# Kernel tuning notes

Measured on AMD Instinct MI355X. Metric: run time of the kernel, lower is better.

Reference implementation:

```python
import jax, jax.numpy as jnp
import numpy as np

B, L, H, V = 256, 200, 128, 50000
NLAYER, K = 2, 20
NEG = -1e10


def setup_inputs() -> dict:
    key = jax.random.key(0)
    ks = jax.random.split(key, 14)
    lens = jax.random.randint(ks[0], (B,), 50, L + 1)
    pos = jnp.arange(L)
    valid = pos[None, :] < lens[:, None]                       # [B,L] bool
    seq = jnp.where(valid, jax.random.randint(ks[1], (B, L), 1, V), 0)
    lengths = valid.astype(jnp.int32)                          # >0 where real token
    reverse_lengths = jnp.where(valid, lens[:, None] - pos[None, :], 0)  # 1..len, 0=pad

    def nrm(k, shape, s=0.02):
        return jax.random.normal(k, shape, jnp.float32) * s

    emb_w = nrm(ks[2], (V, H)).at[0].set(0.0)
    wnoise_w = nrm(ks[3], (L + 1, H)).at[0].set(0.0)
    cluster_w = nrm(ks[4], (L + 1, 1)).at[0].set(0.0)
    ffn1_w = nrm(ks[5], (H, H), 0.05)
    ffn1_b = jnp.zeros((H,), jnp.float32)
    ffn2_w = nrm(ks[6], (H, H), 0.05)
    ffn2_b = jnp.zeros((H,), jnp.float32)
    ln_g = jnp.ones((H,), jnp.float32)
    ln_b = jnp.zeros((H,), jnp.float32)
    gate_w = nrm(ks[7], (2 * H, H), 0.05)
    coff = jax.random.normal(ks[8], (NLAYER, B, L, L), jnp.float32)  # fixed noise (torch.normal)
    return dict(seq=seq, lengths=lengths, reverse_lengths=reverse_lengths,
                emb_w=emb_w, wnoise_w=wnoise_w, cluster_w=cluster_w,
                ffn1_w=ffn1_w, ffn1_b=ffn1_b, ffn2_w=ffn2_w, ffn2_b=ffn2_b,
                ln_g=ln_g, ln_b=ln_b, gate_w=gate_w, coff=coff)


def _sp(x):  # torch.nn.Softplus(threshold=1): identity above 1
    return jnp.where(x > 1.0, x, jnp.log1p(jnp.exp(jnp.minimum(x, 1.0))))


def _forward(seq, lengths, reverse_lengths, emb_w, wnoise_w, cluster_w,
             ffn1_w, ffn1_b, ffn2_w, ffn2_b, ln_g, ln_b, gate_w, coff):
    b, l = seq.shape
    mask = (lengths > 0).astype(jnp.float32)                   # [B,L]
    hidden = emb_w[seq]                                        # [B,L,H]
    slen = jnp.sum(mask, axis=1)                               # [B]
    e_s = hidden[jnp.arange(b), (slen - 1).astype(jnp.int32)]  # last real token state
    zero_layer = jnp.sum(hidden, 1) / slen[:, None]
    layer_collect = [zero_layer]
    eye = jnp.eye(l, dtype=hidden.dtype)
    pair_ok = mask[:, :, None] * mask[:, None, :]              # [B,L,L]
    for i in range(coff.shape[0]):
        wn = wnoise_w[reverse_lengths]                         # [B,L,H]
        sim = jnp.einsum('bld,bmd->blm', hidden, hidden)
        nrm = jnp.linalg.norm(hidden, axis=2, keepdims=True)   # [B,L,1]
        sim = sim / (nrm * nrm.transpose(0, 2, 1) + 1e-6)      # cosine similarity
        diag = cluster_w[reverse_lengths][..., 0]              # [B,L]
        sim = sim + diag[:, :, None] * eye                     # diag_embed add
        sim = sim + coff[i] * _sp(jnp.einsum('bld,bmd->blm', hidden, wn))
        msim = jnp.where(pair_ok == 0.0, NEG, sim)             # masked_fill
        _, idx = jax.lax.top_k(msim, K)                        # [B,L,K]
        sel = jnp.zeros_like(msim).at[jnp.arange(b)[:, None, None],
                                      jnp.arange(l)[None, :, None], idx].set(1.0)
        edges = sel * (msim > NEG).astype(msim.dtype)          # top-k & above-threshold
        cluster_label = edges.transpose(0, 2, 1)
        sim_softmax = jax.nn.softmax(msim, axis=2)
        ssm = cluster_label * sim_softmax                      # [B,L,L] sparse-weighted
        update_hidden = jnp.einsum('blm,bmd->bld', ssm, hidden)
        cmask = jnp.sum(ssm, axis=2)                           # [B,L]
        cmask = cmask / jnp.maximum(jnp.linalg.norm(cmask, axis=1, keepdims=True), 1e-12)
        if i > 0:
            update_hidden = update_hidden * (slen > 1.0).astype(hidden.dtype)[:, None, None]
        feed1 = jax.nn.relu(update_hidden @ ffn1_w + ffn1_b)
        pre = feed1 @ ffn2_w + ffn2_b + update_hidden          # dropout = identity (eval)
        mu = jnp.mean(pre, -1, keepdims=True)
        var = jnp.var(pre, -1, keepdims=True)
        feed2 = (pre - mu) / jnp.sqrt(var + 1e-5) * ln_g + ln_b
        layer_collect.append(jnp.sum(feed2 * cmask[:, :, None], 1))
    e_c = jnp.mean(jnp.stack(layer_collect, 1), 1)             # [B,H]
    alpha = jax.nn.sigmoid(jnp.concatenate([e_c, e_s], -1) @ gate_w)
    sess = alpha * e_c + (1.0 - alpha) * e_s
    scores = sess @ emb_w.T                                    # [B,V]
    return scores


def reference(seq, lengths, reverse_lengths, emb_w, wnoise_w, cluster_w,
              ffn1_w, ffn1_b, ffn2_w, ffn2_b, ln_g, ln_b, gate_w, coff):
    scores = _forward(seq, lengths, reverse_lengths, emb_w, wnoise_w, cluster_w,
                      ffn1_w, ffn1_b, ffn2_w, ffn2_b, ln_g, ln_b, gate_w, coff)
    return (scores, jnp.asarray(0.0, jnp.float32))  # con_loss == 0 when abs=True
```

## Files before the change

kernel.cpp:

```cpp
#include <hip/hip_runtime.h>
#include <cstdint>
#include <cstddef>

namespace {
constexpr int B = 256, L = 200, H = 128, V = 50000, TK = 20;
constexpr int NT = 1563;
constexpr float NEGV = -1e10f;
}

using bf16x8 = __attribute__((ext_vector_type(8))) short;
using s16x8  = __attribute__((ext_vector_type(8))) short;
using f32x16 = __attribute__((ext_vector_type(16))) float;

__device__ inline unsigned short f2bf(float f) {
  unsigned int u = __float_as_uint(f);
  unsigned int r = (u + 0x7fffu + ((u >> 16) & 1u)) >> 16;
  return (unsigned short)r;
}

#define DPP_QUAD_XOR1 0xB1
#define DPP_QUAD_XOR2 0x4E
#define DPP_ROW_HMIRR 0x141
#define DPP_ROW_MIRR  0x140

template <int CTRL>
__device__ inline unsigned dpp16_max_step(unsigned v) {
  unsigned t = (unsigned)__builtin_amdgcn_update_dpp(0, (int)v, CTRL, 0xF, 0xF, true);
  return v > t ? v : t;
}
__device__ inline unsigned grp16_max(unsigned v) {
  v = dpp16_max_step<DPP_QUAD_XOR1>(v);
  v = dpp16_max_step<DPP_QUAD_XOR2>(v);
  v = dpp16_max_step<DPP_ROW_HMIRR>(v);
  v = dpp16_max_step<DPP_ROW_MIRR>(v);
  return v;
}
template <int CTRL>
__device__ inline float dpp16_add_step(float v) {
  int t = __builtin_amdgcn_update_dpp(0, __float_as_int(v), CTRL, 0xF, 0xF, true);
  return v + __int_as_float(t);
}
__device__ inline float grp16_sum(float v) {
  v = dpp16_add_step<DPP_QUAD_XOR1>(v);
  v = dpp16_add_step<DPP_QUAD_XOR2>(v);
  v = dpp16_add_step<DPP_ROW_HMIRR>(v);
  v = dpp16_add_step<DPP_ROW_MIRR>(v);
  return v;
}

__device__ inline unsigned f2key(float f) {
  unsigned b = __float_as_uint(f);
  unsigned m = (unsigned)((int)b >> 31);
  return b ^ (m | 0x80000000u);
}
__device__ inline float key2f(unsigned u) {
  unsigned b = (u & 0x80000000u) ? (u & 0x7fffffffu) : ~u;
  return __uint_as_float(b);
}

__global__ __launch_bounds__(256) void k_embed(const int* __restrict__ seq,
                                               const int* __restrict__ rev,
                                               const float* __restrict__ emb,
                                               const float* __restrict__ wnoise,
                                               float* __restrict__ hidden,
                                               float* __restrict__ nrm,
                                               s16x8* __restrict__ hbh,
                                               s16x8* __restrict__ hbl,
                                               s16x8* __restrict__ wnh,
                                               s16x8* __restrict__ wnl) {
  int b = blockIdx.x / 7, lt = blockIdx.x % 7;
  int t = threadIdx.x;
  int r = t >> 3, c2 = t & 7;
  int l = lt * 32 + r;
  bool valid = l < L;
  float vv[16], wv[16];
  if (valid) {
    int row = b * L + l;
    int tok = seq[row];
    const float4* ep = (const float4*)&emb[(size_t)tok * H + c2 * 16];
    const float4* wp = (const float4*)&wnoise[(size_t)rev[row] * H + c2 * 16];
#pragma unroll
    for (int i = 0; i < 4; ++i) {
      float4 x = ep[i];
      vv[i * 4 + 0] = x.x; vv[i * 4 + 1] = x.y; vv[i * 4 + 2] = x.z; vv[i * 4 + 3] = x.w;
      float4 y = wp[i];
      wv[i * 4 + 0] = y.x; wv[i * 4 + 1] = y.y; wv[i * 4 + 2] = y.z; wv[i * 4 + 3] = y.w;
    }
  } else {
#pragma unroll
    for (int i = 0; i < 16; ++i) { vv[i] = 0.f; wv[i] = 0.f; }
  }
  if (valid) {
    int row = b * L + l;
#pragma unroll
    for (int i = 0; i < 4; ++i)
      *(float4*)&hidden[(size_t)row * H + c2 * 16 + i * 4] =
          make_float4(vv[i * 4], vv[i * 4 + 1], vv[i * 4 + 2], vv[i * 4 + 3]);
    float s = 0.f;
#pragma unroll
    for (int i = 0; i < 16; ++i) s += vv[i] * vv[i];
    s += __shfl_down(s, 4, 8);
    s += __shfl_down(s, 2, 8);
    s += __shfl_down(s, 1, 8);
    if (c2 == 0) nrm[row] = sqrtf(s);
  }
  s16x8 h0, h1, l0, l1, w0, w1, x0, x1;
#pragma unroll
  for (int i = 0; i < 8; ++i) {
    unsigned short hi = f2bf(vv[i]);
    h0[i] = (short)hi;
    l0[i] = (short)f2bf(vv[i] - __uint_as_float((unsigned)hi << 16));
    unsigned short wh = f2bf(wv[i]);
    w0[i] = (short)wh;
    x0[i] = (short)f2bf(wv[i] - __uint_as_float((unsigned)wh << 16));
  }
#pragma unroll
  for (int i = 0; i < 8; ++i) {
    unsigned short hi = f2bf(vv[8 + i]);
    h1[i] = (short)hi;
    l1[i] = (short)f2bf(vv[8 + i] - __uint_as_float((unsigned)hi << 16));
    unsigned short wh = f2bf(wv[8 + i]);
    w1[i] = (short)wh;
    x1[i] = (short)f2bf(wv[8 + i] - __uint_as_float((unsigned)wh << 16));
  }
  size_t fi0 = ((size_t)(b * 7 + lt) * 8 + c2) * 64 + r;
  size_t fi1 = fi0 + 32;
  hbh[fi0] = h0; hbh[fi1] = h1;
  hbl[fi0] = l0; hbl[fi1] = l1;
  wnh[fi0] = w0; wnh[fi1] = w1;
  wnl[fi0] = x0; wnl[fi1] = x1;
}

__global__ __launch_bounds__(512) void k_init(const int* __restrict__ lengths,
                                              const float* __restrict__ hidden,
                                              float* __restrict__ ecacc,
                                              float* __restrict__ e_s) {
  int b = blockIdx.x, tid = threadIdx.x;
  __shared__ float part[4][128];
  __shared__ int wcnt[8];
  __shared__ int s_slen;
  int c = (tid < L && lengths[b * L + tid] > 0) ? 1 : 0;
  for (int o = 32; o > 0; o >>= 1) c += __shfl_down(c, o, 64);
  if ((tid & 63) == 0) wcnt[tid >> 6] = c;
  __syncthreads();
  if (tid == 0) {
    int s = 0;
#pragma unroll
    for (int i = 0; i < 8; ++i) s += wcnt[i];
    s_slen = s;
  }
  int h = tid & 127, seg = tid >> 7;
  float s = 0.f;
  for (int l = seg; l < L; l += 4) s += hidden[(size_t)(b * L + l) * H + h];
  part[seg][h] = s;
  __syncthreads();
  if (tid < 128) {
    float tot = part[0][h] + part[1][h] + part[2][h] + part[3][h];
    int slen = s_slen;
    ecacc[b * H + h] = tot / (float)slen;
    e_s[b * H + h] = hidden[(size_t)(b * L + slen - 1) * H + h];
  }
}

__global__ __launch_bounds__(256) void k_simws(const s16x8* __restrict__ hbh,
                                               const s16x8* __restrict__ hbl,
                                               const s16x8* __restrict__ wnh,
                                               const s16x8* __restrict__ wnl,
                                               const float* __restrict__ nrm,
                                               const int* __restrict__ rev,
                                               const float* __restrict__ cluster,
                                               float* __restrict__ S0,
                                               float* __restrict__ WS) {
  int orig = blockIdx.x;
  int xcd = orig & 7, slot = orig >> 3;
  int b = xcd * 32 + slot / 7, lt = slot % 7;
  int wid = threadIdx.x >> 6, lane = threadIdx.x & 63;
  int lr = lane & 31, kh = lane >> 5;
  size_t abase = ((size_t)(b * 7 + lt) * 8) * 64 + lane;
  bf16x8 ah[8], al[8];
#pragma unroll
  for (int ks = 0; ks < 8; ++ks) {
    ah[ks] = (bf16x8)hbh[abase + ks * 64];
    al[ks] = (bf16x8)hbl[abase + ks * 64];
  }
  for (int mt = wid; mt < 7; mt += 4) {
    size_t bbase = ((size_t)(b * 7 + mt) * 8) * 64 + lane;
    f32x16 accs = {}, accw = {};
#pragma unroll
    for (int ks = 0; ks < 8; ++ks) {
      bf16x8 bhh = (bf16x8)hbh[bbase + ks * 64];
      bf16x8 bhl = (bf16x8)hbl[bbase + ks * 64];
      bf16x8 bwh = (bf16x8)wnh[bbase + ks * 64];
      bf16x8 bwl = (bf16x8)wnl[bbase + ks * 64];
      accs = __builtin_amdgcn_mfma_f32_32x32x16_bf16(ah[ks], bhh, accs, 0, 0, 0);
      accs = __builtin_amdgcn_mfma_f32_32x32x16_bf16(ah[ks], bhl, accs, 0, 0, 0);
      accs = __builtin_amdgcn_mfma_f32_32x32x16_bf16(al[ks], bhh, accs, 0, 0, 0);
      accw = __builtin_amdgcn_mfma_f32_32x32x16_bf16(ah[ks], bwh, accw, 0, 0, 0);
      accw = __builtin_amdgcn_mfma_f32_32x32x16_bf16(ah[ks], bwl, accw, 0, 0, 0);
      accw = __builtin_amdgcn_mfma_f32_32x32x16_bf16(al[ks], bwh, accw, 0, 0, 0);
    }
    int m = mt * 32 + lr;
    if (m < L) {
      float nm = nrm[b * L + m];
#pragma unroll
      for (int r = 0; r < 16; ++r) {
        int row = lt * 32 + (r & 3) + 8 * (r >> 2) + 4 * kh;
        if (row < L) {
          float nl = nrm[b * L + row];
          float s0 = accs[r] * __builtin_amdgcn_rcpf(nl * nm + 1e-6f);
          if (row == m) s0 += cluster[rev[b * L + row]];
          size_t o = (size_t)(b * L + row) * L + m;
          S0[o] = s0;
          float x = accw[r];
          WS[o] = (x > 1.f) ? x : __logf(1.f + __expf(x));
        }
      }
    }
  }
}

__global__ __launch_bounds__(256) void k_rowpass(const float* __restrict__ S0,
                                                 const float* __restrict__ WS,
                                                 const float* __restrict__ coff_i,
                                                 const int* __restrict__ lengths,
                                                 float* __restrict__ P,
                                                 unsigned char* __restrict__ ET) {
  int wid = threadIdx.x >> 6, lane = threadIdx.x & 63;
  int g = lane >> 4, q = lane & 15;
  int bb = blockIdx.x / 13, blk = blockIdx.x % 13;
  int l = blk * 16 + wid * 4 + g;
  bool lvalid = l < L;
  int lrow = bb * L + (lvalid ? l : 0);
  bool mask_l = lvalid && (lengths[lrow] > 0);
  size_t base = (size_t)lrow * L;
  float val[13]; unsigned key[13]; unsigned vmask = 0;
#pragma unroll
  for (int j = 0; j < 13; ++j) {
    int m = q + 16 * j;
    float v = 0.f; bool ok = false;
    if (mask_l && m < L) {
      ok = lengths[bb * L + m] > 0;
      if (ok) v = S0[base + m] + coff_i[base + m] * WS[base + m];
    }
    val[j] = v;
    key[j] = ok ? f2key(v) : 0u;
    vmask |= ok ? (1u << j) : 0u;
  }
  unsigned Mu = 0u;
  for (int t = 0; t < TK; ++t) {
    unsigned lv = key[0]; int lj = 0;
#pragma unroll
    for (int j = 1; j < 13; ++j) {
      bool gt = key[j] > lv;
      lv = gt ? key[j] : lv;
      lj = gt ? j : lj;
    }
    unsigned gm = grp16_max(lv);
    if (t == 0) Mu = gm;
    if (__all(gm == 0u)) break;
    unsigned long long bal = __ballot(lv == gm && gm != 0u);
    unsigned long long mine = bal & (0xFFFFull << (g * 16));
    int owner = mine ? (int)__builtin_ctzll(mine) : -1;
    bool is_owner = (lane == owner);
    if (is_owner) {
      int m = q + 16 * lj;
      ET[((size_t)bb * L + m) * L + l] = 1;
    }
#pragma unroll
    for (int j = 0; j < 13; ++j) key[j] = (is_owner && lj == j) ? 0u : key[j];
  }
  float M = key2f(Mu);
  float e[13]; float s = 0.f;
#pragma unroll
  for (int j = 0; j < 13; ++j) {
    float ev = ((vmask >> j) & 1u) ? __expf(val[j] - M) : 0.f;
    e[j] = ev; s += ev;
  }
  s = grp16_sum(s);
  float inv = (s > 0.f) ? __builtin_amdgcn_rcpf(s) : 0.f;
  if (lvalid) {
#pragma unroll
    for (int j = 0; j < 13; ++j) {
      int m = q + 16 * j;
      if (m < L) P[base + m] = e[j] * inv;
    }
  }
}

__global__ __launch_bounds__(256) void k_compact(float* __restrict__ P,
                                                 unsigned char* __restrict__ ET,
                                                 float* __restrict__ cmask,
                                                 int* __restrict__ cnt) {
  int wid = threadIdx.x >> 6, lane = threadIdx.x & 63;
  int row = blockIdx.x * 4 + wid;
  size_t base = (size_t)row * L;
  float w[4];
  float s = 0.f;
#pragma unroll
  for (int j = 0; j < 4; ++j) {
    int m = lane + 64 * j;
    float ww = 0.f;
    if (m < L) ww = P[base + m] * (float)ET[base + m];
    w[j] = ww; s += ww;
  }
  float ssum = s;
  for (int off = 1; off < 64; off <<= 1) ssum += __shfl_xor(ssum, off, 64);
  if (lane == 0) cmask[row] = ssum;
  int pos_base = 0;
#pragma unroll
  for (int j = 0; j < 4; ++j) {
    bool nz = (w[j] != 0.f);
    unsigned long long mk = __ballot(nz);
    int rank = __popcll(mk & ((1ull << lane) - 1ull));
    if (nz) {
      int pos = pos_base + rank;
      ET[base + pos] = (unsigned char)(lane + 64 * j);
      P[base + pos] = w[j];
    }
    pos_base += (int)__popcll(mk);
  }
  if (lane == 0) cnt[row] = pos_base;
}

__global__ __launch_bounds__(64) void k_cnorm(float* __restrict__ cmask) {
  int b = blockIdx.x, lane = threadIdx.x;
  float v[4]; float s = 0.f;
#pragma unroll
  for (int j = 0; j < 4; ++j) {
    int l = lane + 64 * j;
    float x = (l < L) ? cmask[b * L + l] : 0.f;
    v[j] = x; s += x * x;
  }
  for (int off = 1; off < 64; off <<= 1) s += __shfl_xor(s, off, 64);
  float inv = 1.f / fmaxf(sqrtf(s), 1e-12f);
#pragma unroll
  for (int j = 0; j < 4; ++j) {
    int l = lane + 64 * j;
    if (l < L) cmask[b * L + l] = v[j] * inv;
  }
}

__global__ __launch_bounds__(256) void k_update(const float* __restrict__ P,
                                                const unsigned char* __restrict__ ET,
                                                const int* __restrict__ cnt,
                                                const float* __restrict__ hidden,
                                                float* __restrict__ upd) {
  int row = blockIdx.x * 2 + (threadIdx.x >> 7);
  int h = threadIdx.x & 127;
  int b = row / L;
  size_t base = (size_t)row * L;
  int n = cnt[row];
  float acc = 0.f;
  for (int e0 = 0; e0 < n; e0 += TK) {
    float w[TK]; int m[TK];
    float4 p4[5];
#pragma unroll
    for (int i = 0; i < 5; ++i) p4[i] = *(const float4*)&P[base + e0 + i * 4];
#pragma unroll
    for (int i = 0; i < 5; ++i) {
      w[i * 4 + 0] = p4[i].x; w[i * 4 + 1] = p4[i].y;
      w[i * 4 + 2] = p4[i].z; w[i * 4 + 3] = p4[i].w;
    }
#pragma unroll
    for (int e = 0; e < TK; ++e) m[e] = ET[base + e0 + e];
    float hv[TK];
#pragma unroll
    for (int e = 0; e < TK; ++e)
      hv[e] = hidden[(size_t)(b * L + m[e]) * H + h];
#pragma unroll
    for (int e = 0; e < TK; ++e)
      acc += ((e0 + e) < n ? w[e] : 0.f) * hv[e];
  }
  upd[(size_t)row * H + h] = acc;
}

__global__ __launch_bounds__(256) void k_ffn(float* __restrict__ upd,
                                             const float* __restrict__ W1,
                                             const float* __restrict__ b1,
                                             const float* __restrict__ W2,
                                             const float* __restrict__ b2,
                                             const float* __restrict__ g,
                                             const float* __restrict__ beta,
                                             const float* __restrict__ cmask) {
  constexpr int AS = 136;
  __shared__ __align__(16) char smem[4 * 64 * AS * 2];
  short* ahs = (short*)smem;
  short* als = ahs + 64 * AS;
  short* f1h = (short*)(smem + 2 * 64 * AS * 2);
  short* f1l = f1h + 64 * AS;
  float (*ps)[132] = (float (*)[132])smem;
  __shared__ float mus[64], rsd[64];
  int row0 = blockIdx.x * 64;
  int tid = threadIdx.x;
  int wid = tid >> 6, lane = tid & 63;
  int lr = lane & 31, kh = lane >> 5;
  int n0 = wid * 32;
  int n = n0 + lr;
#pragma unroll
  for (int it = 0; it < 8; ++it) {
    int f = it * 256 + tid;
    int r = f >> 5, c4 = (f & 31) * 4;
    float4 v = *(const float4*)&upd[(size_t)(row0 + r) * H + c4];
    float vv[4] = {v.x, v.y, v.z, v.w};
    unsigned short hh[4]; short ll[4];
#pragma unroll
    for (int q2 = 0; q2 < 4; ++q2) {
      hh[q2] = f2bf(vv[q2]);
      ll[q2] = (short)f2bf(vv[q2] - __uint_as_float((unsigned)hh[q2] << 16));
    }
    uint2 ph = make_uint2((unsigned)hh[0] | ((unsigned)hh[1] << 16),
                          (unsigned)hh[2] | ((unsigned)hh[3] << 16));
    uint2 pl = make_uint2((unsigned short)ll[0] | ((unsigned)(unsigned short)ll[1] << 16),
                          (unsigned short)ll[2] | ((unsigned)(unsigned short)ll[3] << 16));
    *(uint2*)&ahs[r * AS + c4] = ph;
    *(uint2*)&als[r * AS + c4] = pl;
  }
  __syncthreads();
  bf16x8 wfh[8], wfl[8];
#pragma unroll
  for (int ks = 0; ks < 8; ++ks) {
#pragma unroll
    for (int i = 0; i < 8; ++i) {
      float w = W1[(size_t)(ks * 16 + kh * 8 + i) * H + n];
      unsigned short hi = f2bf(w);
      wfh[ks][i] = (short)hi;
      wfl[ks][i] = (short)f2bf(w - __uint_as_float((unsigned)hi << 16));
    }
  }
  f32x16 acc0, acc1;
  {
    float bv = b1[n];
#pragma unroll
    for (int r = 0; r < 16; ++r) { acc0[r] = bv; acc1[r] = bv; }
  }
#pragma unroll
  for (int ks = 0; ks < 8; ++ks) {
    bf16x8 xh0 = *(const bf16x8*)&ahs[(0 * 32 + lr) * AS + ks * 16 + kh * 8];
    bf16x8 xl0 = *(const bf16x8*)&als[(0 * 32 + lr) * AS + ks * 16 + kh * 8];
    bf16x8 xh1 = *(const bf16x8*)&ahs[(1 * 32 + lr) * AS + ks * 16 + kh * 8];
    bf16x8 xl1 = *(const bf16x8*)&als[(1 * 32 + lr) * AS + ks * 16 + kh * 8];
    acc0 = __builtin_amdgcn_mfma_f32_32x32x16_bf16(xh0, wfh[ks], acc0, 0, 0, 0);
    acc0 = __builtin_amdgcn_mfma_f32_32x32x16_bf16(xl0, wfh[ks], acc0, 0, 0, 0);
    acc0 = __builtin_amdgcn_mfma_f32_32x32x16_bf16(xh0, wfl[ks], acc0, 0, 0, 0);
    acc1 = __builtin_amdgcn_mfma_f32_32x32x16_bf16(xh1, wfh[ks], acc1, 0, 0, 0);
    acc1 = __builtin_amdgcn_mfma_f32_32x32x16_bf16(xl1, wfh[ks], acc1, 0, 0, 0);
    acc1 = __builtin_amdgcn_mfma_f32_32x32x16_bf16(xh1, wfl[ks], acc1, 0, 0, 0);
  }
#pragma unroll
  for (int r = 0; r < 16; ++r) {
    int crow = (r & 3) + 8 * (r >> 2) + 4 * kh;
    float f0 = fmaxf(acc0[r], 0.f);
    unsigned short h0 = f2bf(f0);
    f1h[crow * AS + n] = (short)h0;
    f1l[crow * AS + n] = (short)f2bf(f0 - __uint_as_float((unsigned)h0 << 16));
    float f1v = fmaxf(acc1[r], 0.f);
    unsigned short h1 = f2bf(f1v);
    f1h[(32 + crow) * AS + n] = (short)h1;
    f1l[(32 + crow) * AS + n] = (short)f2bf(f1v - __uint_as_float((unsigned)h1 << 16));
  }
  __syncthreads();
#pragma unroll
  for (int ks = 0; ks < 8; ++ks) {
#pragma unroll
    for (int i = 0; i < 8; ++i) {
      float w = W2[(size_t)(ks * 16 + kh * 8 + i) * H + n];
      unsigned short hi = f2bf(w);
      wfh[ks][i] = (short)hi;
      wfl[ks][i] = (short)f2bf(w - __uint_as_float((unsigned)hi << 16));
    }
  }
  {
    float bv = b2[n];
#pragma unroll
    for (int r = 0; r < 16; ++r) { acc0[r] = bv; acc1[r] = bv; }
  }
#pragma unroll
  for (int ks = 0; ks < 8; ++ks) {
    bf16x8 xh0 = *(const bf16x8*)&f1h[(0 * 32 + lr) * AS + ks * 16 + kh * 8];
    bf16x8 xl0 = *(const bf16x8*)&f1l[(0 * 32 + lr) * AS + ks * 16 + kh * 8];
    bf16x8 xh1 = *(const bf16x8*)&f1h[(1 * 32 + lr) * AS + ks * 16 + kh * 8];
    bf16x8 xl1 = *(const bf16x8*)&f1l[(1 * 32 + lr) * AS + ks * 16 + kh * 8];
    acc0 = __builtin_amdgcn_mfma_f32_32x32x16_bf16(xh0, wfh[ks], acc0, 0, 0, 0);
    acc0 = __builtin_amdgcn_mfma_f32_32x32x16_bf16(xl0, wfh[ks], acc0, 0, 0, 0);
    acc0 = __builtin_amdgcn_mfma_f32_32x32x16_bf16(xh0, wfl[ks], acc0, 0, 0, 0);
    acc1 = __builtin_amdgcn_mfma_f32_32x32x16_bf16(xh1, wfh[ks], acc1, 0, 0, 0);
    acc1 = __builtin_amdgcn_mfma_f32_32x32x16_bf16(xl1, wfh[ks], acc1, 0, 0, 0);
    acc1 = __builtin_amdgcn_mfma_f32_32x32x16_bf16(xh1, wfl[ks], acc1, 0, 0, 0);
  }
#pragma unroll
  for (int r = 0; r < 16; ++r) {
    int crow = (r & 3) + 8 * (r >> 2) + 4 * kh;
    float p0 = acc0[r] + upd[(size_t)(row0 + crow) * H + n];
    float p1 = acc1[r] + upd[(size_t)(row0 + 32 + crow) * H + n];
    acc0[r] = p0; acc1[r] = p1;
    ps[crow][n] = p0;
    ps[32 + crow][n] = p1;
  }
  __syncthreads();
  {
    int r = tid >> 2, sub = tid & 3;
    float s = 0.f, sq = 0.f;
#pragma unroll
    for (int j = 0; j < 8; ++j) {
      float4 x = *(const float4*)&ps[r][sub * 32 + j * 4];
      s += x.x + x.y + x.z + x.w;
      sq += x.x * x.x + x.y * x.y + x.z * x.z + x.w * x.w;
    }
    s += __shfl_down(s, 2, 4);  s += __shfl_down(s, 1, 4);
    sq += __shfl_down(sq, 2, 4); sq += __shfl_down(sq, 1, 4);
    if (sub == 0) {
      float mu = s * (1.f / 128.f);
      float var = sq * (1.f / 128.f) - mu * mu;
      mus[r] = mu;
      rsd[r] = rsqrtf(var + 1e-5f);
    }
  }
  __syncthreads();
  {
    float gn = g[n], bn = beta[n];
#pragma unroll
    for (int r = 0; r < 16; ++r) {
      int crow = (r & 3) + 8 * (r >> 2) + 4 * kh;
      float o0 = ((acc0[r] - mus[crow]) * rsd[crow] * gn + bn) * cmask[row0 + crow];
      float o1 = ((acc1[r] - mus[32 + crow]) * rsd[32 + crow] * gn + bn) * cmask[row0 + 32 + crow];
      upd[(size_t)(row0 + crow) * H + n] = o0;
      upd[(size_t)(row0 + 32 + crow) * H + n] = o1;
    }
  }
}

__global__ __launch_bounds__(512) void k_ecadd(const float* __restrict__ wf,
                                               float* __restrict__ ecacc) {
  int b = blockIdx.x, tid = threadIdx.x;
  __shared__ float part[4][128];
  int h = tid & 127, seg = tid >> 7;
  float s = 0.f;
  for (int l = seg; l < L; l += 4) s += wf[(size_t)(b * L + l) * H + h];
  part[seg][h] = s;
  __syncthreads();
  if (tid < 128)
    ecacc[b * H + h] += part[0][h] + part[1][h] + part[2][h] + part[3][h];
}

__global__ __launch_bounds__(256) void k_embconv(const float* __restrict__ emb,
                                                 s16x8* __restrict__ ebh,
                                                 s16x8* __restrict__ ebl) {
  int nt = blockIdx.x;
  int t = threadIdx.x;
  int r = t >> 3, c2 = t & 7;
  int n = nt * 32 + r;
  float vv[16];
  if (n < V) {
    const float4* ep = (const float4*)&emb[(size_t)n * H + c2 * 16];
#pragma unroll
    for (int i = 0; i < 4; ++i) {
      float4 x = ep[i];
      vv[i * 4 + 0] = x.x; vv[i * 4 + 1] = x.y; vv[i * 4 + 2] = x.z; vv[i * 4 + 3] = x.w;
    }
  } else {
#pragma unroll
    for (int i = 0; i < 16; ++i) vv[i] = 0.f;
  }
  s16x8 h0, h1, l0, l1;
#pragma unroll
  for (int i = 0; i < 8; ++i) {
    unsigned short hi = f2bf(vv[i]);
    h0[i] = (short)hi;
    l0[i] = (short)f2bf(vv[i] - __uint_as_float((unsigned)hi << 16));
    unsigned short hj = f2bf(vv[8 + i]);
    h1[i] = (short)hj;
    l1[i] = (short)f2bf(vv[8 + i] - __uint_as_float((unsigned)hj << 16));
  }
  size_t fi0 = ((size_t)nt * 8 + c2) * 64 + r;
  size_t fi1 = fi0 + 32;
  ebh[fi0] = h0; ebh[fi1] = h1;
  ebl[fi0] = l0; ebl[fi1] = l1;
}

__global__ __launch_bounds__(128) void k_gate(const float* __restrict__ ecacc,
                                              const float* __restrict__ e_s,
                                              const float* __restrict__ gw,
                                              float* __restrict__ sess,
                                              float* __restrict__ out) {
  __shared__ float cat[256];
  int b = blockIdx.x, h = threadIdx.x;
  float ec = ecacc[b * H + h] * (1.f / 3.f);
  float es = e_s[b * H + h];
  cat[h] = ec; cat[128 + h] = es;
  __syncthreads();
  float a = 0.f;
  for (int j = 0; j < 256; ++j) a = fmaf(cat[j], gw[(size_t)j * H + h], a);
  a = 1.f / (1.f + __expf(-a));
  sess[b * H + h] = a * ec + (1.f - a) * es;
  if (b == 0 && h == 0) out[(size_t)B * V] = 0.f;
}

__global__ __launch_bounds__(256) void k_scores(const float* __restrict__ sess,
                                                const s16x8* __restrict__ ebh,
                                                const s16x8* __restrict__ ebl,
                                                float* __restrict__ out) {
  int wid = threadIdx.x >> 6, lane = threadIdx.x & 63;
  int lr = lane & 31, kh = lane >> 5;
  int mt = blockIdx.y;
  int m = mt * 32 + lr;
  bf16x8 ah[8], al[8];
#pragma unroll
  for (int ks = 0; ks < 8; ++ks) {
    const float* sp = &sess[(size_t)m * H + ks * 16 + kh * 8];
    float4 a = *(const float4*)sp;
    float4 c = *(const float4*)(sp + 4);
    float av[8] = {a.x, a.y, a.z, a.w, c.x, c.y, c.z, c.w};
#pragma unroll
    for (int i = 0; i < 8; ++i) {
      unsigned short hi = f2bf(av[i]);
      ah[ks][i] = (short)hi;
      al[ks][i] = (short)f2bf(av[i] - __uint_as_float((unsigned)hi << 16));
    }
  }
  int ntEnd = min(blockIdx.x * 16 + 16, NT);
  for (int nt = blockIdx.x * 16 + wid; nt < ntEnd; nt += 4) {
    size_t bbase = ((size_t)nt * 8) * 64 + lane;
    f32x16 acc = {};
#pragma unroll
    for (int ks = 0; ks < 8; ++ks) {
      bf16x8 bh = (bf16x8)ebh[bbase + ks * 64];
      bf16x8 bl = (bf16x8)ebl[bbase + ks * 64];
      acc = __builtin_amdgcn_mfma_f32_32x32x16_bf16(ah[ks], bh, acc, 0, 0, 0);
      acc = __builtin_amdgcn_mfma_f32_32x32x16_bf16(al[ks], bh, acc, 0, 0, 0);
      acc = __builtin_amdgcn_mfma_f32_32x32x16_bf16(ah[ks], bl, acc, 0, 0, 0);
    }
    int n = nt * 32 + lr;
    if (n < V) {
#pragma unroll
      for (int r = 0; r < 16; ++r) {
        int row = mt * 32 + (r & 3) + 8 * (r >> 2) + 4 * kh;
        out[(size_t)row * V + n] = acc[r];
      }
    }
  }
}

extern "C" void kernel_launch(void* const* d_in, const int* in_sizes, int n_in,
                              void* d_out, int out_size, void* d_ws, size_t ws_size,
                              hipStream_t stream) {
  const int*   seq  = (const int*)d_in[0];
  const int*   lens = (const int*)d_in[1];
  const int*   rev  = (const int*)d_in[2];
  const float* emb  = (const float*)d_in[3];
  const float* wnz  = (const float*)d_in[4];
  const float* clw  = (const float*)d_in[5];
  const float* w1   = (const float*)d_in[6];
  const float* fb1  = (const float*)d_in[7];
  const float* w2   = (const float*)d_in[8];
  const float* fb2  = (const float*)d_in[9];
  const float* lng  = (const float*)d_in[10];
  const float* lnb  = (const float*)d_in[11];
  const float* gw   = (const float*)d_in[12];
  const float* coff = (const float*)d_in[13];
  float* out = (float*)d_out;

  char* ws = (char*)d_ws;
  size_t off = 0;
  auto alloc = [&](size_t bytes) {
    void* p = ws + off;
    off += (bytes + 255) & ~(size_t)255;
    return p;
  };
  float* hidden = (float*)alloc((size_t)B * L * H * 4);
  float* nrm    = (float*)alloc((size_t)B * L * 4);
  float* S0     = (float*)alloc((size_t)B * L * L * 4);
  float* WS     = (float*)alloc((size_t)B * L * L * 4);
  float* P      = (float*)alloc((size_t)B * L * L * 4);
  float* upd    = (float*)alloc((size_t)B * L * H * 4);
  float* cmask  = (float*)alloc((size_t)B * L * 4);
  int*   cnt    = (int*)alloc((size_t)B * L * 4);
  float* e_s    = (float*)alloc((size_t)B * H * 4);
  float* ecacc  = (float*)alloc((size_t)B * H * 4);
  float* sess   = (float*)alloc((size_t)B * H * 4);
  unsigned char* ET = (unsigned char*)alloc((size_t)B * L * L);
  s16x8* hbh = (s16x8*)alloc((size_t)B * 7 * 8 * 64 * 16);
  s16x8* wnh = (s16x8*)alloc((size_t)B * 7 * 8 * 64 * 16);
  s16x8* hbl = (s16x8*)P;
  s16x8* wnl = (s16x8*)upd;
  s16x8* ebh = (s16x8*)S0;
  s16x8* ebl = (s16x8*)WS;

  k_embed<<<B * 7, 256, 0, stream>>>(seq, rev, emb, wnz, hidden, nrm,
                                     hbh, hbl, wnh, wnl);
  k_init<<<B, 512, 0, stream>>>(lens, hidden, ecacc, e_s);
  k_simws<<<B * 7, 256, 0, stream>>>(hbh, hbl, wnh, wnl, nrm, rev, clw, S0, WS);

  for (int i = 0; i < 2; ++i) {
    hipMemsetAsync(ET, 0, (size_t)B * L * L, stream);
    k_rowpass<<<B * 13, 256, 0, stream>>>(S0, WS, coff + (size_t)i * B * L * L,
                                          lens, P, ET);
    k_compact<<<B * L / 4, 256, 0, stream>>>(P, ET, cmask, cnt);
    k_cnorm<<<B, 64, 0, stream>>>(cmask);
    k_update<<<B * L / 2, 256, 0, stream>>>(P, ET, cnt, hidden, upd);
    k_ffn<<<B * L / 64, 256, 0, stream>>>(upd, w1, fb1, w2, fb2, lng, lnb, cmask);
    k_ecadd<<<B, 512, 0, stream>>>(upd, ecacc);
  }

  k_embconv<<<NT, 256, 0, stream>>>(emb, ebh, ebl);
  k_gate<<<B, 128, 0, stream>>>(ecacc, e_s, gw, sess, out);
  k_scores<<<dim3((NT + 15) / 16, 8), 256, 0, stream>>>(sess, ebh, ebl, out);
}
```

Baseline: 475.3 us.

## Fuse similarity/weight computation with per-row top-k softmax for both layers

Merges the similarity/softplus MFMA kernel with the row pass so the S0 and WS tiles stay in shared memory instead of round-tripping through global memory. The row pass for both layers is computed up front in the fused kernel, writing separate P and ET buffers per layer, and both ET buffers are zeroed before the loop. This removes two full B*L*L float writes and several reads plus kernel launches, at the cost of about 53KB of shared memory per block (lower occupancy) and a serialized top-k phase inside the MFMA kernel. Workspace aliasing is reshuffled to fit the extra buffers.

```diff
diff --git a/kernel.cpp b/kernel.cpp
--- a/kernel.cpp
+++ b/kernel.cpp
@@ -162,15 +162,21 @@
   }
 }
 
-__global__ __launch_bounds__(256) void k_simws(const s16x8* __restrict__ hbh,
+__global__ __launch_bounds__(256) void k_fused(const s16x8* __restrict__ hbh,
                                                const s16x8* __restrict__ hbl,
                                                const s16x8* __restrict__ wnh,
                                                const s16x8* __restrict__ wnl,
                                                const float* __restrict__ nrm,
                                                const int* __restrict__ rev,
                                                const float* __restrict__ cluster,
-                                               float* __restrict__ S0,
-                                               float* __restrict__ WS) {
+                                               const int* __restrict__ lengths,
+                                               const float* __restrict__ coff,
+                                               float* __restrict__ P1,
+                                               float* __restrict__ P2,
+                                               unsigned char* __restrict__ ET1,
+                                               unsigned char* __restrict__ ET2) {
+  __shared__ float s0l[32][208];
+  __shared__ float wsl[32][208];
   int orig = blockIdx.x;
   int xcd = orig & 7, slot = orig >> 3;
   int b = xcd * 32 + slot / 7, lt = slot % 7;
@@ -204,85 +210,85 @@
       float nm = nrm[b * L + m];
 #pragma unroll
       for (int r = 0; r < 16; ++r) {
-        int row = lt * 32 + (r & 3) + 8 * (r >> 2) + 4 * kh;
+        int ri = (r & 3) + 8 * (r >> 2) + 4 * kh;
+        int row = lt * 32 + ri;
         if (row < L) {
           float nl = nrm[b * L + row];
           float s0 = accs[r] * __builtin_amdgcn_rcpf(nl * nm + 1e-6f);
           if (row == m) s0 += cluster[rev[b * L + row]];
-          size_t o = (size_t)(b * L + row) * L + m;
-          S0[o] = s0;
+          s0l[ri][m] = s0;
           float x = accw[r];
-          WS[o] = (x > 1.f) ? x : __logf(1.f + __expf(x));
+          wsl[ri][m] = (x > 1.f) ? x : __logf(1.f + __expf(x));
         }
       }
     }
   }
-}
-
-__global__ __launch_bounds__(256) void k_rowpass(const float* __restrict__ S0,
-                                                 const float* __restrict__ WS,
-                                                 const float* __restrict__ coff_i,
-                                                 const int* __restrict__ lengths,
-                                                 float* __restrict__ P,
-                                                 unsigned char* __restrict__ ET) {
-  int wid = threadIdx.x >> 6, lane = threadIdx.x & 63;
+  __syncthreads();
   int g = lane >> 4, q = lane & 15;
-  int bb = blockIdx.x / 13, blk = blockIdx.x % 13;
-  int l = blk * 16 + wid * 4 + g;
-  bool lvalid = l < L;
-  int lrow = bb * L + (lvalid ? l : 0);
-  bool mask_l = lvalid && (lengths[lrow] > 0);
-  size_t base = (size_t)lrow * L;
-  float val[13]; unsigned key[13]; unsigned vmask = 0;
-#pragma unroll
-  for (int j = 0; j < 13; ++j) {
-    int m = q + 16 * j;
-    float v = 0.f; bool ok = false;
-    if (mask_l && m < L) {
-      ok = lengths[bb * L + m] > 0;
-      if (ok) v = S0[base + m] + coff_i[base + m] * WS[base + m];
-    }
-    val[j] = v;
-    key[j] = ok ? f2key(v) : 0u;
-    vmask |= ok ? (1u << j) : 0u;
-  }
-  unsigned Mu = 0u;
-  for (int t = 0; t < TK; ++t) {
-    unsigned lv = key[0]; int lj = 0;
-#pragma unroll
-    for (int j = 1; j < 13; ++j) {
-      bool gt = key[j] > lv;
-      lv = gt ? key[j] : lv;
-      lj = gt ? j : lj;
-    }
-    unsigned gm = grp16_max(lv);
-    if (t == 0) Mu = gm;
-    if (__all(gm == 0u)) break;
-    unsigned long long bal = __ballot(lv == gm && gm != 0u);
-    unsigned long long mine = bal & (0xFFFFull << (g * 16));
-    int owner = mine ? (int)__builtin_ctzll(mine) : -1;
-    bool is_owner = (lane == owner);
-    if (is_owner) {
-      int m = q + 16 * lj;
-      ET[((size_t)bb * L + m) * L + l] = 1;
-    }
-#pragma unroll
-    for (int j = 0; j < 13; ++j) key[j] = (is_owner && lj == j) ? 0u : key[j];
-  }
-  float M = key2f(Mu);
-  float e[13]; float s = 0.f;
-#pragma unroll
-  for (int j = 0; j < 13; ++j) {
-    float ev = ((vmask >> j) & 1u) ? __expf(val[j] - M) : 0.f;
-    e[j] = ev; s += ev;
-  }
-  s = grp16_sum(s);
-  float inv = (s > 0.f) ? __builtin_amdgcn_rcpf(s) : 0.f;
-  if (lvalid) {
-#pragma unroll
-    for (int j = 0; j < 13; ++j) {
-      int m = q + 16 * j;
-      if (m < L) P[base + m] = e[j] * inv;
+  int g16 = wid * 4 + g;
+  for (int i = 0; i < 2; ++i) {
+    const float* coff_i = coff + (size_t)i * B * L * L;
+    float* P = i ? P2 : P1;
+    unsigned char* ET = i ? ET2 : ET1;
+    for (int rr = 0; rr < 2; ++rr) {
+      int ri = rr * 16 + g16;
+      int l = lt * 32 + ri;
+      bool lvalid = l < L;
+      int lrow = b * L + (lvalid ? l : 0);
+      bool mask_l = lvalid && (lengths[lrow] > 0);
+      size_t base = (size_t)lrow * L;
+      float val[13]; unsigned key[13]; unsigned vmask = 0;
+#pragma unroll
+      for (int j = 0; j < 13; ++j) {
+        int m = q + 16 * j;
+        float v = 0.f; bool ok = false;
+        if (mask_l && m < L) {
+          ok = lengths[b * L + m] > 0;
+          if (ok) v = s0l[ri][m] + coff_i[base + m] * wsl[ri][m];
+        }
+        val[j] = v;
+        key[j] = ok ? f2key(v) : 0u;
+        vmask |= ok ? (1u << j) : 0u;
+      }
+      unsigned Mu = 0u;
+      for (int t = 0; t < TK; ++t) {
+        unsigned lv = key[0]; int lj = 0;
+#pragma unroll
+        for (int j = 1; j < 13; ++j) {
+          bool gt = key[j] > lv;
+          lv = gt ? key[j] : lv;
+          lj = gt ? j : lj;
+        }
+        unsigned gm = grp16_max(lv);
+        if (t == 0) Mu = gm;
+        if (__all(gm == 0u)) break;
+        unsigned long long bal = __ballot(lv == gm && gm != 0u);
+        unsigned long long mine = bal & (0xFFFFull << (g * 16));
+        int owner = mine ? (int)__builtin_ctzll(mine) : -1;
+        bool is_owner = (lane == owner);
+        if (is_owner) {
+          int m = q + 16 * lj;
+          ET[((size_t)b * L + m) * L + l] = 1;
+        }
+#pragma unroll
+        for (int j = 0; j < 13; ++j) key[j] = (is_owner && lj == j) ? 0u : key[j];
+      }
+      float M = key2f(Mu);
+      float e[13]; float s = 0.f;
+#pragma unroll
+      for (int j = 0; j < 13; ++j) {
+        float ev = ((vmask >> j) & 1u) ? __expf(val[j] - M) : 0.f;
+        e[j] = ev; s += ev;
+      }
+      s = grp16_sum(s);
+      float inv = (s > 0.f) ? __builtin_amdgcn_rcpf(s) : 0.f;
+      if (lvalid) {
+#pragma unroll
+        for (int j = 0; j < 13; ++j) {
+          int m = q + 16 * j;
+          if (m < L) P[base + m] = e[j] * inv;
+        }
+      }
     }
   }
 }
@@ -668,32 +674,34 @@
   };
   float* hidden = (float*)alloc((size_t)B * L * H * 4);
   float* nrm    = (float*)alloc((size_t)B * L * 4);
-  float* S0     = (float*)alloc((size_t)B * L * L * 4);
-  float* WS     = (float*)alloc((size_t)B * L * L * 4);
-  float* P      = (float*)alloc((size_t)B * L * L * 4);
+  float* P1     = (float*)alloc((size_t)B * L * L * 4);
+  float* P2     = (float*)alloc((size_t)B * L * L * 4);
   float* upd    = (float*)alloc((size_t)B * L * H * 4);
   float* cmask  = (float*)alloc((size_t)B * L * 4);
   int*   cnt    = (int*)alloc((size_t)B * L * 4);
   float* e_s    = (float*)alloc((size_t)B * H * 4);
   float* ecacc  = (float*)alloc((size_t)B * H * 4);
   float* sess   = (float*)alloc((size_t)B * H * 4);
-  unsigned char* ET = (unsigned char*)alloc((size_t)B * L * L);
+  unsigned char* ET1 = (unsigned char*)alloc((size_t)B * L * L);
+  unsigned char* ET2 = (unsigned char*)alloc((size_t)B * L * L);
   s16x8* hbh = (s16x8*)alloc((size_t)B * 7 * 8 * 64 * 16);
   s16x8* wnh = (s16x8*)alloc((size_t)B * 7 * 8 * 64 * 16);
-  s16x8* hbl = (s16x8*)P;
-  s16x8* wnl = (s16x8*)upd;
-  s16x8* ebh = (s16x8*)S0;
-  s16x8* ebl = (s16x8*)WS;
+  s16x8* wnl = (s16x8*)alloc((size_t)B * 7 * 8 * 64 * 16);
+  s16x8* hbl = (s16x8*)upd;
+  s16x8* ebh = (s16x8*)P1;
+  s16x8* ebl = (s16x8*)P2;
 
   k_embed<<<B * 7, 256, 0, stream>>>(seq, rev, emb, wnz, hidden, nrm,
                                      hbh, hbl, wnh, wnl);
   k_init<<<B, 512, 0, stream>>>(lens, hidden, ecacc, e_s);
-  k_simws<<<B * 7, 256, 0, stream>>>(hbh, hbl, wnh, wnl, nrm, rev, clw, S0, WS);
+  hipMemsetAsync(ET1, 0, (size_t)B * L * L, stream);
+  hipMemsetAsync(ET2, 0, (size_t)B * L * L, stream);
+  k_fused<<<B * 7, 256, 0, stream>>>(hbh, hbl, wnh, wnl, nrm, rev, clw,
+                                     lens, coff, P1, P2, ET1, ET2);
 
   for (int i = 0; i < 2; ++i) {
-    hipMemsetAsync(ET, 0, (size_t)B * L * L, stream);
-    k_rowpass<<<B * 13, 256, 0, stream>>>(S0, WS, coff + (size_t)i * B * L * L,
-                                          lens, P, ET);
+    float* P = i ? P2 : P1;
+    unsigned char* ET = i ? ET2 : ET1;
     k_compact<<<B * L / 4, 256, 0, stream>>>(P, ET, cmask, cnt);
     k_cnorm<<<B, 64, 0, stream>>>(cmask);
     k_update<<<B * L / 2, 256, 0, stream>>>(P, ET, cnt, hidden, upd);
```

Measured after the change: 486.0 us. 2.3% more time.
